# Kernel optimization log

Measured on AMD Instinct MI355X. Metric: run time of the kernel, lower is better.

Reference implementation:

```python
import jax, jax.numpy as jnp
import numpy as np

M, K, N, E = 8192, 1024, 1024, 8  # total tokens, in-dim, out-dim, experts/segments


def setup_inputs() -> dict:
    key = jax.random.key(0)
    k1, k2, k3 = jax.random.split(key, 3)
    a = jax.random.normal(k1, (M, K), dtype=jnp.float32)
    b = jax.random.normal(k2, (E, N, K), dtype=jnp.float32) * 0.02  # column-major per-expert weights
    c = jnp.zeros((M, N), dtype=jnp.float32)
    inner = jnp.sort(jax.random.randint(k3, (E - 1,), 0, M, dtype=jnp.int32))
    seg_indptr = jnp.concatenate([
        jnp.zeros((1,), jnp.int32), inner, jnp.full((1,), M, jnp.int32)
    ])  # [E+1], monotone, covers [0, M)
    weight_indices = jnp.arange(E, dtype=jnp.int32)
    return {
        "a": a, "b": b, "c": c,
        "batch_size": E, "weight_column_major": 1,
        "seg_indptr": seg_indptr, "weight_indices": weight_indices,
    }


def reference(a, b, c, batch_size, weight_column_major, seg_indptr, weight_indices):
    # Grouped GEMM: for each contiguous segment s of rows [seg_indptr[s], seg_indptr[s+1]),
    # c[rows] = a[rows] @ b[weight_indices[s]].T  (b is [E, N, K], column-major weights).
    assert weight_column_major
    rows = jnp.arange(a.shape[0])[:, None]  # [M, 1]
    out = c
    for s in range(batch_size):  # fixed small loop over experts/segments
        b_e = jnp.take(b, weight_indices[s], axis=0)  # [N, K]
        seg_out = a @ b_e.T                            # [M, N]
        mask = (rows >= seg_indptr[s]) & (rows < seg_indptr[s + 1])
        out = jnp.where(mask, seg_out, out)
    return out
```

## Files before the change

kernel.cpp:

```cpp
#include <hip/hip_runtime.h>
#include <hip/hip_bf16.h>
#include <stdint.h>

#define MDIM 8192
#define KDIM 1024
#define NDIM 1024
#define NEXP 8
#define BM 128
#define BN 128
#define BK 32

typedef __attribute__((ext_vector_type(8))) short bf16x8;
typedef __attribute__((ext_vector_type(4))) float floatx4;

#if __has_builtin(__builtin_amdgcn_cvt_pk_bf16_f32)
typedef __attribute__((ext_vector_type(2))) __bf16 bf16x2v;
static __device__ __forceinline__ int cvt2(float x, float y) {
    bf16x2v r = __builtin_amdgcn_cvt_pk_bf16_f32(x, y);
    return __builtin_bit_cast(int, r);
}
#else
static __device__ __forceinline__ unsigned short f2b(float f) {
    unsigned int u = __float_as_uint(f);
    return (unsigned short)((u + 0x7fffu + ((u >> 16) & 1u)) >> 16);
}
static __device__ __forceinline__ int cvt2(float x, float y) {
    return (int)f2b(x) | ((int)f2b(y) << 16);
}
#endif

static __device__ __forceinline__ bf16x8 pack8(float4 a, float4 b) {
    int4 r;
    r.x = cvt2(a.x, a.y);
    r.y = cvt2(a.z, a.w);
    r.z = cvt2(b.x, b.y);
    r.w = cvt2(b.z, b.w);
    return __builtin_bit_cast(bf16x8, r);
}

#define GLDS(gp, lp) __builtin_amdgcn_global_load_lds(                        \
    (const __attribute__((address_space(1))) unsigned int*)(gp),              \
    (__attribute__((address_space(3))) unsigned int*)(lp), 16, 0, 0)

__global__ __launch_bounds__(256, 2)
void grouped_gemm_f32(const float* __restrict__ A,
                      const float* __restrict__ B,
                      const int* __restrict__ seg_indptr,
                      const int* __restrict__ widx,
                      float* __restrict__ c)
{
    __shared__ float As0[BM * BK], As1[BM * BK];
    __shared__ float Bs0[BN * BK], Bs1[BN * BK];

    const int bid = ((int)blockIdx.x & 7) * 71 + ((int)blockIdx.x >> 3);

    const int NTN = NDIM / BN;
    int rem = bid;
    int s = -1, m0 = 0, seg_end = 0, n0 = 0;
    for (int i = 0; i < NEXP; ++i) {
        int ps = seg_indptr[i], pe = seg_indptr[i + 1];
        int nt = ((pe - ps + BM - 1) / BM) * NTN;
        if (rem < nt) { s = i; m0 = ps + (rem / NTN) * BM; n0 = (rem % NTN) * BN; seg_end = pe; break; }
        rem -= nt;
    }
    if (s < 0) return;

    const float* __restrict__ be = B + (size_t)widx[s] * (size_t)(NDIM * KDIM);

    const int tid  = (int)threadIdx.x;
    const int wave = tid >> 6;
    const int lane = tid & 63;

    const int srow = tid >> 3;
    const int gch  = ((tid & 7) ^ (srow & 7)) * 4;
    const float* ap[4];
    const float* bp[4];
#pragma unroll
    for (int j = 0; j < 4; ++j) {
        int ra = m0 + j * 32 + srow; if (ra >= MDIM) ra = MDIM - 1;
        ap[j] = A  + (size_t)ra * KDIM + gch;
        bp[j] = be + (size_t)(n0 + j * 32 + srow) * KDIM + gch;
    }
    const int ldso = wave * 256;

    const int wm = (wave & 1) * 64;
    const int wn = (wave >> 1) * 64;
    const int fr   = lane & 15;
    const int quad = lane >> 4;
    const int p0 = ((2 * quad) ^ (fr & 7)) * 4;
    const int p1 = ((2 * quad + 1) ^ (fr & 7)) * 4;

    floatx4 acc[4][4] = {};

#define STAGE(AS, BS, kk)                                                     \
    do {                                                                      \
        _Pragma("unroll")                                                     \
        for (int j = 0; j < 4; ++j) {                                         \
            GLDS(ap[j] + (kk), &AS[j * 1024 + ldso]);                         \
            GLDS(bp[j] + (kk), &BS[j * 1024 + ldso]);                         \
        }                                                                     \
    } while (0)

#define COMPUTE(AS, BS)                                                       \
    do {                                                                      \
        bf16x8 af[4], bf[4];                                                  \
        _Pragma("unroll")                                                     \
        for (int mi = 0; mi < 4; ++mi) {                                      \
            const int base = (wm + mi * 16 + fr) * BK;                        \
            af[mi] = pack8(*reinterpret_cast<const float4*>(&AS[base + p0]),  \
                           *reinterpret_cast<const float4*>(&AS[base + p1])); \
        }                                                                     \
        _Pragma("unroll")                                                     \
        for (int ni = 0; ni < 4; ++ni) {                                      \
            const int base = (wn + ni * 16 + fr) * BK;                        \
            bf[ni] = pack8(*reinterpret_cast<const float4*>(&BS[base + p0]),  \
                           *reinterpret_cast<const float4*>(&BS[base + p1])); \
        }                                                                     \
        _Pragma("unroll")                                                     \
        for (int mi = 0; mi < 4; ++mi)                                        \
            _Pragma("unroll")                                                 \
            for (int ni = 0; ni < 4; ++ni)                                    \
                acc[mi][ni] = __builtin_amdgcn_mfma_f32_16x16x32_bf16(        \
                    af[mi], bf[ni], acc[mi][ni], 0, 0, 0);                    \
    } while (0)

    STAGE(As0, Bs0, 0);
#pragma unroll 1
    for (int ii = 0; ii < 16; ++ii) {
        const int i0 = ii * 2;
        __syncthreads();
        STAGE(As1, Bs1, (i0 + 1) * BK);
        COMPUTE(As0, Bs0);
        __syncthreads();
        if (i0 + 2 < 32) STAGE(As0, Bs0, (i0 + 2) * BK);
        COMPUTE(As1, Bs1);
    }

#pragma unroll
    for (int mi = 0; mi < 4; ++mi) {
        const int rbase = m0 + wm + mi * 16 + quad * 4;
#pragma unroll
        for (int ni = 0; ni < 4; ++ni) {
            const int col = n0 + wn + ni * 16 + fr;
#pragma unroll
            for (int j = 0; j < 4; ++j) {
                const int row = rbase + j;
                if (row < seg_end)
                    c[(size_t)row * NDIM + col] = acc[mi][ni][j];
            }
        }
    }
#undef STAGE
#undef COMPUTE
}

extern "C" void kernel_launch(void* const* d_in, const int* in_sizes, int n_in,
                              void* d_out, int out_size, void* d_ws, size_t ws_size,
                              hipStream_t stream) {
    const float* a          = (const float*)d_in[0];
    const float* b          = (const float*)d_in[1];
    const int*   seg_indptr = (const int*)d_in[5];
    const int*   widx       = (const int*)d_in[6];
    float*       out        = (float*)d_out;

    hipLaunchKernelGGL(grouped_gemm_f32, dim3(568), dim3(256), 0, stream,
                       a, b, seg_indptr, widx, out);
}
```

Measured before the change: 193.8 us.

## Pre-convert inputs to bf16 and use persistent work-stealing grouped GEMM

Adds a separate kernel that converts A and all expert weights from fp32 to bf16 in workspace, so the GEMM streams half the bytes and skips in-loop packing. BK grows to 64 to match the smaller element size. The GEMM becomes persistent with a 512-block grid that takes extra tiles through an atomic counter, which rebalances uneven segments. In exchange it pays an extra pass over A and B, a memset, and an atomic per tile.

Result: faster. 172.5 us (-10.9%).

```diff
diff --git a/kernel.cpp b/kernel.cpp
--- a/kernel.cpp
+++ b/kernel.cpp
@@ -8,34 +8,33 @@
 #define NEXP 8
 #define BM 128
 #define BN 128
-#define BK 32
+#define BK 64
+#define PGRID 512
 
 typedef __attribute__((ext_vector_type(8))) short bf16x8;
 typedef __attribute__((ext_vector_type(4))) float floatx4;
+typedef __attribute__((ext_vector_type(8))) unsigned short ushort8;
 
-#if __has_builtin(__builtin_amdgcn_cvt_pk_bf16_f32)
-typedef __attribute__((ext_vector_type(2))) __bf16 bf16x2v;
-static __device__ __forceinline__ int cvt2(float x, float y) {
-    bf16x2v r = __builtin_amdgcn_cvt_pk_bf16_f32(x, y);
-    return __builtin_bit_cast(int, r);
-}
-#else
 static __device__ __forceinline__ unsigned short f2b(float f) {
     unsigned int u = __float_as_uint(f);
     return (unsigned short)((u + 0x7fffu + ((u >> 16) & 1u)) >> 16);
 }
-static __device__ __forceinline__ int cvt2(float x, float y) {
-    return (int)f2b(x) | ((int)f2b(y) << 16);
-}
-#endif
 
-static __device__ __forceinline__ bf16x8 pack8(float4 a, float4 b) {
-    int4 r;
-    r.x = cvt2(a.x, a.y);
-    r.y = cvt2(a.z, a.w);
-    r.z = cvt2(b.x, b.y);
-    r.w = cvt2(b.z, b.w);
-    return __builtin_bit_cast(bf16x8, r);
+__global__ __launch_bounds__(256)
+void cvt_bf16(const float* __restrict__ a, const float* __restrict__ b,
+              unsigned short* __restrict__ wa, unsigned short* __restrict__ wb)
+{
+    const long t  = (long)blockIdx.x * 256 + threadIdx.x;
+    const long NA = (long)MDIM * KDIM / 8;
+    const float* src; unsigned short* dst; long v;
+    if (t < NA) { src = a; dst = wa; v = t; }
+    else        { src = b; dst = wb; v = t - NA; }
+    const float4 lo = ((const float4*)src)[2 * v];
+    const float4 hi = ((const float4*)src)[2 * v + 1];
+    ushort8 o;
+    o[0] = f2b(lo.x); o[1] = f2b(lo.y); o[2] = f2b(lo.z); o[3] = f2b(lo.w);
+    o[4] = f2b(hi.x); o[5] = f2b(hi.y); o[6] = f2b(hi.z); o[7] = f2b(hi.w);
+    ((ushort8*)dst)[v] = o;
 }
 
 #define GLDS(gp, lp) __builtin_amdgcn_global_load_lds(                        \
@@ -43,115 +42,124 @@
     (__attribute__((address_space(3))) unsigned int*)(lp), 16, 0, 0)
 
 __global__ __launch_bounds__(256, 2)
-void grouped_gemm_f32(const float* __restrict__ A,
-                      const float* __restrict__ B,
-                      const int* __restrict__ seg_indptr,
-                      const int* __restrict__ widx,
-                      float* __restrict__ c)
+void grouped_gemm_v7(const unsigned short* __restrict__ A,
+                     const unsigned short* __restrict__ B,
+                     const int* __restrict__ seg_indptr,
+                     const int* __restrict__ widx,
+                     float* __restrict__ c,
+                     int* __restrict__ steal_cnt)
 {
-    __shared__ float As0[BM * BK], As1[BM * BK];
-    __shared__ float Bs0[BN * BK], Bs1[BN * BK];
-
-    const int bid = ((int)blockIdx.x & 7) * 71 + ((int)blockIdx.x >> 3);
-
-    const int NTN = NDIM / BN;
-    int rem = bid;
-    int s = -1, m0 = 0, seg_end = 0, n0 = 0;
-    for (int i = 0; i < NEXP; ++i) {
-        int ps = seg_indptr[i], pe = seg_indptr[i + 1];
-        int nt = ((pe - ps + BM - 1) / BM) * NTN;
-        if (rem < nt) { s = i; m0 = ps + (rem / NTN) * BM; n0 = (rem % NTN) * BN; seg_end = pe; break; }
-        rem -= nt;
-    }
-    if (s < 0) return;
-
-    const float* __restrict__ be = B + (size_t)widx[s] * (size_t)(NDIM * KDIM);
+    __shared__ unsigned short As0[BM * BK], As1[BM * BK];
+    __shared__ unsigned short Bs0[BN * BK], Bs1[BN * BK];
 
     const int tid  = (int)threadIdx.x;
     const int wave = tid >> 6;
     const int lane = tid & 63;
-
     const int srow = tid >> 3;
-    const int gch  = ((tid & 7) ^ (srow & 7)) * 4;
-    const float* ap[4];
-    const float* bp[4];
-#pragma unroll
-    for (int j = 0; j < 4; ++j) {
-        int ra = m0 + j * 32 + srow; if (ra >= MDIM) ra = MDIM - 1;
-        ap[j] = A  + (size_t)ra * KDIM + gch;
-        bp[j] = be + (size_t)(n0 + j * 32 + srow) * KDIM + gch;
-    }
-    const int ldso = wave * 256;
-
-    const int wm = (wave & 1) * 64;
-    const int wn = (wave >> 1) * 64;
+    const int gch  = ((tid & 7) ^ (srow & 7)) * 8;
+    const int ldso = wave * 512;
+    const int wm   = (wave & 1) * 64;
+    const int wn   = (wave >> 1) * 64;
     const int fr   = lane & 15;
     const int quad = lane >> 4;
-    const int p0 = ((2 * quad) ^ (fr & 7)) * 4;
-    const int p1 = ((2 * quad + 1) ^ (fr & 7)) * 4;
+    const int fro0 = ((0 * 4 + quad) ^ (fr & 7)) * 8;
+    const int fro1 = ((1 * 4 + quad) ^ (fr & 7)) * 8;
 
-    floatx4 acc[4][4] = {};
+    int ntiles = 0;
+#pragma unroll
+    for (int i = 0; i < NEXP; ++i)
+        ntiles += ((seg_indptr[i + 1] - seg_indptr[i] + BM - 1) / BM) * (NDIM / BN);
+
+    __shared__ int next_tile_sh;
+
+    int tile = (int)blockIdx.x;
+    while (tile < ntiles) {
+        int rem = tile, s = 0, m0 = 0, seg_end = 0, n0 = 0;
+        for (int i = 0; i < NEXP; ++i) {
+            int ps = seg_indptr[i], pe = seg_indptr[i + 1];
+            int nt = ((pe - ps + BM - 1) / BM) * (NDIM / BN);
+            if (rem < nt) { s = i; m0 = ps + (rem / (NDIM / BN)) * BM; n0 = (rem % (NDIM / BN)) * BN; seg_end = pe; break; }
+            rem -= nt;
+        }
+        const unsigned short* __restrict__ be = B + (size_t)widx[s] * (size_t)(NDIM * KDIM);
+
+        const unsigned short* ap[4];
+        const unsigned short* bp[4];
+#pragma unroll
+        for (int j = 0; j < 4; ++j) {
+            int ra = m0 + j * 32 + srow; if (ra >= MDIM) ra = MDIM - 1;
+            ap[j] = A  + (size_t)ra * KDIM + gch;
+            bp[j] = be + (size_t)(n0 + j * 32 + srow) * KDIM + gch;
+        }
+
+        floatx4 acc[4][4] = {};
 
 #define STAGE(AS, BS, kk)                                                     \
-    do {                                                                      \
-        _Pragma("unroll")                                                     \
-        for (int j = 0; j < 4; ++j) {                                         \
-            GLDS(ap[j] + (kk), &AS[j * 1024 + ldso]);                         \
-            GLDS(bp[j] + (kk), &BS[j * 1024 + ldso]);                         \
-        }                                                                     \
-    } while (0)
+        do {                                                                  \
+            _Pragma("unroll")                                                 \
+            for (int j = 0; j < 4; ++j) {                                     \
+                GLDS(ap[j] + (kk), &AS[j * 2048 + ldso]);                     \
+                GLDS(bp[j] + (kk), &BS[j * 2048 + ldso]);                     \
+            }                                                                 \
+        } while (0)
 
 #define COMPUTE(AS, BS)                                                       \
-    do {                                                                      \
-        bf16x8 af[4], bf[4];                                                  \
-        _Pragma("unroll")                                                     \
-        for (int mi = 0; mi < 4; ++mi) {                                      \
-            const int base = (wm + mi * 16 + fr) * BK;                        \
-            af[mi] = pack8(*reinterpret_cast<const float4*>(&AS[base + p0]),  \
-                           *reinterpret_cast<const float4*>(&AS[base + p1])); \
-        }                                                                     \
-        _Pragma("unroll")                                                     \
-        for (int ni = 0; ni < 4; ++ni) {                                      \
-            const int base = (wn + ni * 16 + fr) * BK;                        \
-            bf[ni] = pack8(*reinterpret_cast<const float4*>(&BS[base + p0]),  \
-                           *reinterpret_cast<const float4*>(&BS[base + p1])); \
-        }                                                                     \
-        _Pragma("unroll")                                                     \
-        for (int mi = 0; mi < 4; ++mi)                                        \
+        do {                                                                  \
+            bf16x8 af[4], bf[4];                                              \
             _Pragma("unroll")                                                 \
-            for (int ni = 0; ni < 4; ++ni)                                    \
-                acc[mi][ni] = __builtin_amdgcn_mfma_f32_16x16x32_bf16(        \
-                    af[mi], bf[ni], acc[mi][ni], 0, 0, 0);                    \
-    } while (0)
+            for (int h = 0; h < 2; ++h) {                                     \
+                const int fro = h ? fro1 : fro0;                              \
+                _Pragma("unroll")                                             \
+                for (int mi = 0; mi < 4; ++mi)                                \
+                    af[mi] = *reinterpret_cast<const bf16x8*>(                \
+                        &AS[(wm + mi * 16 + fr) * BK + fro]);                 \
+                _Pragma("unroll")                                             \
+                for (int ni = 0; ni < 4; ++ni)                                \
+                    bf[ni] = *reinterpret_cast<const bf16x8*>(                \
+                        &BS[(wn + ni * 16 + fr) * BK + fro]);                 \
+                _Pragma("unroll")                                             \
+                for (int mi = 0; mi < 4; ++mi)                                \
+                    _Pragma("unroll")                                         \
+                    for (int ni = 0; ni < 4; ++ni)                            \
+                        acc[mi][ni] = __builtin_amdgcn_mfma_f32_16x16x32_bf16(\
+                            af[mi], bf[ni], acc[mi][ni], 0, 0, 0);            \
+            }                                                                 \
+        } while (0)
 
-    STAGE(As0, Bs0, 0);
+        STAGE(As0, Bs0, 0);
 #pragma unroll 1
-    for (int ii = 0; ii < 16; ++ii) {
-        const int i0 = ii * 2;
-        __syncthreads();
-        STAGE(As1, Bs1, (i0 + 1) * BK);
-        COMPUTE(As0, Bs0);
-        __syncthreads();
-        if (i0 + 2 < 32) STAGE(As0, Bs0, (i0 + 2) * BK);
-        COMPUTE(As1, Bs1);
-    }
+        for (int ii = 0; ii < 8; ++ii) {
+            const int i0 = ii * 2;
+            __syncthreads();
+            STAGE(As1, Bs1, (i0 + 1) * BK);
+            COMPUTE(As0, Bs0);
+            __syncthreads();
+            if (i0 + 2 < 16) STAGE(As0, Bs0, (i0 + 2) * BK);
+            COMPUTE(As1, Bs1);
+        }
+
+        if (tid == 0)
+            next_tile_sh = PGRID + atomicAdd(steal_cnt, 1);
 
 #pragma unroll
-    for (int mi = 0; mi < 4; ++mi) {
-        const int rbase = m0 + wm + mi * 16 + quad * 4;
+        for (int mi = 0; mi < 4; ++mi) {
+            const int rbase = m0 + wm + mi * 16 + quad * 4;
 #pragma unroll
-        for (int ni = 0; ni < 4; ++ni) {
-            const int col = n0 + wn + ni * 16 + fr;
+            for (int ni = 0; ni < 4; ++ni) {
+                const int col = n0 + wn + ni * 16 + fr;
 #pragma unroll
-            for (int j = 0; j < 4; ++j) {
-                const int row = rbase + j;
-                if (row < seg_end)
-                    c[(size_t)row * NDIM + col] = acc[mi][ni][j];
+                for (int j = 0; j < 4; ++j) {
+                    const int row = rbase + j;
+                    if (row < seg_end)
+                        c[(size_t)row * NDIM + col] = acc[mi][ni][j];
+                }
             }
         }
-    }
+        __syncthreads();
+        tile = next_tile_sh;
 #undef STAGE
 #undef COMPUTE
+    }
 }
 
 extern "C" void kernel_launch(void* const* d_in, const int* in_sizes, int n_in,
@@ -163,6 +171,12 @@
     const int*   widx       = (const int*)d_in[6];
     float*       out        = (float*)d_out;
 
-    hipLaunchKernelGGL(grouped_gemm_f32, dim3(568), dim3(256), 0, stream,
-                       a, b, seg_indptr, widx, out);
+    unsigned short* wa  = (unsigned short*)d_ws;
+    unsigned short* wb  = wa + (size_t)MDIM * KDIM;
+    int*            cnt = (int*)(wb + (size_t)NEXP * NDIM * KDIM);
+
+    hipMemsetAsync(cnt, 0, sizeof(int), stream);
+    hipLaunchKernelGGL(cvt_bf16, dim3(8192), dim3(256), 0, stream, a, b, wa, wb);
+    hipLaunchKernelGGL(grouped_gemm_v7, dim3(PGRID), dim3(256), 0, stream,
+                       wa, wb, seg_indptr, widx, out, cnt);
 }
```
